# Kernel tuning notes

Hardware: AMD Instinct MI355X
Metric: run time of the kernel (lower is better)

Reference implementation:

```python
import jax, jax.numpy as jnp
import numpy as np

PATCH_SIZES = [4, 8, 16]
B, S, D, H = 32, 1000, 64, 512


def setup_inputs() -> dict:
    key = jax.random.key(0)
    ks = jax.random.split(key, 8)
    inp = {"x": jax.random.normal(ks[0], (B, S, D), dtype=jnp.float32)}
    for i, p in enumerate(PATCH_SIZES):
        fan_in = p * D
        inp[f"W{i}"] = jax.random.normal(ks[1 + 2 * i], (H, fan_in), dtype=jnp.float32) / np.sqrt(fan_in).astype(np.float32)
        inp[f"b{i}"] = jax.random.normal(ks[2 + 2 * i], (H,), dtype=jnp.float32) * 0.01
    inp["pos"] = jax.random.normal(ks[7], (1, 1000, H), dtype=jnp.float32)
    return inp


def reference(x, W0, b0, W1, b1, W2, b2, pos):
    Ws = [W0, W1, W2]
    bs = [b0, b1, b2]
    batch, seq_len, d = x.shape
    min_len = seq_len - max(PATCH_SIZES) + 1  # all scales truncated to this
    embs = []
    for p, W, b in zip(PATCH_SIZES, Ws, bs):
        # sliding windows, stride 1, only the first min_len windows are kept
        idx = jnp.arange(min_len)[:, None] + jnp.arange(p)[None, :]  # (min_len, p)
        win = x[:, idx, :]  # (batch, min_len, p, d) -- im2col gather
        # torch Linear on flattened [time, feature] patch: W[h, t*d + f]
        Wk = W.reshape(-1, p, d)  # (H, p, d)
        embs.append(jnp.einsum('blpd,hpd->blh', win, Wk) + b)
    out = jnp.stack(embs, axis=1).mean(axis=1)  # mean over scales
    return out + pos[:, :min_len, :]
```

## Files before the change

kernel.cpp:

```cpp
#include <hip/hip_runtime.h>
#include <stdint.h>

typedef unsigned short u16;
typedef __attribute__((ext_vector_type(8))) short bf16x8;
typedef __attribute__((ext_vector_type(8))) u16  u16x8;
typedef __attribute__((ext_vector_type(4))) float f32x4;

static constexpr int BATCH  = 32;
static constexpr int SEQ    = 1000;
static constexpr int DIM    = 64;
static constexpr int HOUT   = 512;
static constexpr int MINLEN = 985;
static constexpr int KTOT   = 1024;
static constexpr int AROWS  = 288;

static constexpr size_t XB_OFF   = 0;
static constexpr size_t WF_OFF   = 4u << 20;
static constexpr size_t BE_OFF   = 5u << 20;
static constexpr int    XB_TOTAL = 2048000 + 4096;

__device__ inline u16 f2bf(float f) {
  union { float f; uint32_t u; } v; v.f = f;
  uint32_t r = v.u + 0x7fffu + ((v.u >> 16) & 1u);
  return (u16)(r >> 16);
}

__global__ void pe_prep_x(const float* __restrict__ x, u16* __restrict__ xb) {
  int i = (blockIdx.x * 256 + threadIdx.x) * 8;
  if (i >= XB_TOTAL) return;
  u16x8 o;
  if (i < 2048000) {
    const float4* p = (const float4*)(x + i);
    float4 a = p[0], c = p[1];
    o[0] = f2bf(a.x); o[1] = f2bf(a.y); o[2] = f2bf(a.z); o[3] = f2bf(a.w);
    o[4] = f2bf(c.x); o[5] = f2bf(c.y); o[6] = f2bf(c.z); o[7] = f2bf(c.w);
  } else {
    o = (u16x8)(0);
  }
  *(u16x8*)(xb + i) = o;
}

__global__ void pe_prep_w(const float* __restrict__ W0, const float* __restrict__ W1,
                          const float* __restrict__ W2, const float* __restrict__ b0,
                          const float* __restrict__ b1, const float* __restrict__ b2,
                          u16* __restrict__ Wf, float* __restrict__ beff) {
  int i = blockIdx.x * 256 + threadIdx.x;
  if (i < HOUT * KTOT) {
    int h = i >> 10, j = i & 1023;
    float e = W2[i];
    if (j < 512) e += W1[(h << 9) + j];
    if (j < 256) e += W0[(h << 8) + j];
    Wf[i] = f2bf(e * (1.0f / 3.0f));
  } else if (i < HOUT * KTOT + HOUT) {
    int h = i - HOUT * KTOT;
    beff[h] = (b0[h] + b1[h] + b2[h]) * (1.0f / 3.0f);
  }
}

__device__ inline void gload_lds16(const void* g, void* l) {
  __builtin_amdgcn_global_load_lds(
      (const __attribute__((address_space(1))) uint32_t*)g,
      (__attribute__((address_space(3))) uint32_t*)l, 16, 0, 0);
}

__global__ __launch_bounds__(512, 4) void pe_gemm(
    const u16* __restrict__ xb, const u16* __restrict__ Wf,
    const float* __restrict__ beff, const float* __restrict__ pos,
    float* __restrict__ out) {
  __shared__ u16 ldsA[AROWS * 64];
  __shared__ u16 ldsB[2][128 * 64];

  const int t    = threadIdx.x;
  const int w    = t >> 6;
  const int lane = t & 63;
  const int b    = blockIdx.z;
  const int l0   = blockIdx.y * 256;
  const int n0   = blockIdx.x * 128;
  const int wr   = w >> 1;
  const int wc   = w & 1;
  const int lr   = lane & 15;
  const int g    = lane >> 4;

  const int srow = lane >> 3;
  const int scol = ((lane & 7) ^ (lane >> 3)) * 8;

  const u16* Ab = xb + b * (SEQ * DIM) + l0 * 64;
  const u16* Bb = Wf + (size_t)n0 * KTOT;

  #pragma unroll
  for (int i = 0; i < 4; ++i) {
    int c = w * 4 + i;
    gload_lds16(Ab + (c * 8 + srow) * 64 + scol, &ldsA[c * 512]);
  }
  if (w < 4) {
    int c = 32 + w;
    gload_lds16(Ab + (c * 8 + srow) * 64 + scol, &ldsA[c * 512]);
  }
  #pragma unroll
  for (int i = 0; i < 2; ++i) {
    int c = w * 2 + i;
    gload_lds16(Bb + (size_t)(c * 8 + srow) * KTOT + scol, &ldsB[0][c * 512]);
  }
  __syncthreads();

  f32x4 acc[4][4] = {};
  int cur = 0;

  for (int kt = 0; kt < 16; ++kt) {
    if (kt < 15) {
      #pragma unroll
      for (int i = 0; i < 2; ++i) {
        int c = w * 2 + i;
        gload_lds16(Bb + (size_t)(c * 8 + srow) * KTOT + (kt + 1) * 64 + scol,
                    &ldsB[cur ^ 1][c * 512]);
      }
    }
    #pragma unroll
    for (int kk = 0; kk < 2; ++kk) {
      bf16x8 aF[4], bF[4];
      #pragma unroll
      for (int m = 0; m < 4; ++m) {
        int r = wr * 64 + m * 16 + lr + kt;
        aF[m] = *(const bf16x8*)&ldsA[r * 64 + ((kk * 4 + g) ^ (r & 7)) * 8];
      }
      #pragma unroll
      for (int n = 0; n < 4; ++n) {
        int r = wc * 64 + n * 16 + lr;
        bF[n] = *(const bf16x8*)&ldsB[cur][r * 64 + ((kk * 4 + g) ^ (r & 7)) * 8];
      }
      #pragma unroll
      for (int m = 0; m < 4; ++m)
        #pragma unroll
        for (int n = 0; n < 4; ++n)
          acc[m][n] = __builtin_amdgcn_mfma_f32_16x16x32_bf16(aF[m], bF[n], acc[m][n], 0, 0, 0);
    }
    __syncthreads();
    cur ^= 1;
  }

  #pragma unroll
  for (int n = 0; n < 4; ++n) {
    const int h  = n0 + wc * 64 + n * 16 + lr;
    const float bv = beff[h];
    #pragma unroll
    for (int m = 0; m < 4; ++m) {
      const int rowb = l0 + wr * 64 + m * 16 + (g << 2);
      #pragma unroll
      for (int r = 0; r < 4; ++r) {
        const int l = rowb + r;
        if (l < MINLEN) {
          out[((size_t)b * MINLEN + l) * HOUT + h] =
              acc[m][n][r] + bv + pos[(size_t)l * HOUT + h];
        }
      }
    }
  }
}

extern "C" void kernel_launch(void* const* d_in, const int* in_sizes, int n_in,
                              void* d_out, int out_size, void* d_ws, size_t ws_size,
                              hipStream_t stream) {
  const float* x   = (const float*)d_in[0];
  const float* W0  = (const float*)d_in[1];
  const float* b0  = (const float*)d_in[2];
  const float* W1  = (const float*)d_in[3];
  const float* b1  = (const float*)d_in[4];
  const float* W2  = (const float*)d_in[5];
  const float* b2  = (const float*)d_in[6];
  const float* pos = (const float*)d_in[7];
  float* out = (float*)d_out;

  char* ws  = (char*)d_ws;
  u16*  xbf = (u16*)(ws + XB_OFF);
  u16*  Wf  = (u16*)(ws + WF_OFF);
  float* be = (float*)(ws + BE_OFF);

  hipLaunchKernelGGL(pe_prep_x, dim3(XB_TOTAL / (256 * 8)), dim3(256), 0, stream, x, xbf);
  hipLaunchKernelGGL(pe_prep_w, dim3((HOUT * KTOT + HOUT) / 256), dim3(256), 0, stream,
                     W0, W1, W2, b0, b1, b2, Wf, be);
  hipLaunchKernelGGL(pe_gemm, dim3(HOUT / 128, 4, BATCH), dim3(512), 0, stream,
                     xbf, Wf, be, pos, out);
}
```

Baseline: 58.02 us.

## Widen GEMM N-tile to 256 with triple-buffered B loads and interleaved barriers

Doubles the per-block output tile width from 128 to 256 columns, so each block computes 4x8 MFMA accumulators and the grid shrinks by half. The B operand becomes triple-buffered with a prefetch distance of two k-steps. Global-to-LDS loads are split into quarter chunks interleaved with MFMA phases, using explicit waitcnt/barrier and setprio to overlap memory with compute. This raises reuse of the A (shifted window) tile and hides load latency, at the cost of more registers and LDS, lower occupancy (launch bounds 2), and only 256 blocks on a large-CU GPU.

Measured after the change: 74.47 us. +28.3%, slower.

```diff
diff --git a/kernel.cpp b/kernel.cpp
--- a/kernel.cpp
+++ b/kernel.cpp
@@ -13,6 +13,7 @@
 static constexpr int MINLEN = 985;
 static constexpr int KTOT   = 1024;
 static constexpr int AROWS  = 288;
+static constexpr int BUF    = 256 * 64;
 
 static constexpr size_t XB_OFF   = 0;
 static constexpr size_t WF_OFF   = 4u << 20;
@@ -63,26 +64,26 @@
       (__attribute__((address_space(3))) uint32_t*)l, 16, 0, 0);
 }
 
-__global__ __launch_bounds__(512, 4) void pe_gemm(
+__global__ __launch_bounds__(512, 2) void pe_gemm(
     const u16* __restrict__ xb, const u16* __restrict__ Wf,
     const float* __restrict__ beff, const float* __restrict__ pos,
     float* __restrict__ out) {
   __shared__ u16 ldsA[AROWS * 64];
-  __shared__ u16 ldsB[2][128 * 64];
+  __shared__ u16 ldsB[3 * BUF];
 
   const int t    = threadIdx.x;
   const int w    = t >> 6;
   const int lane = t & 63;
   const int b    = blockIdx.z;
   const int l0   = blockIdx.y * 256;
-  const int n0   = blockIdx.x * 128;
+  const int n0   = blockIdx.x * 256;
   const int wr   = w >> 1;
   const int wc   = w & 1;
   const int lr   = lane & 15;
   const int g    = lane >> 4;
 
   const int srow = lane >> 3;
-  const int scol = ((lane & 7) ^ (lane >> 3)) * 8;
+  const int scol = ((lane & 7) ^ srow) * 8;
 
   const u16* Ab = xb + b * (SEQ * DIM) + l0 * 64;
   const u16* Bb = Wf + (size_t)n0 * KTOT;
@@ -97,50 +98,79 @@
     gload_lds16(Ab + (c * 8 + srow) * 64 + scol, &ldsA[c * 512]);
   }
   #pragma unroll
-  for (int i = 0; i < 2; ++i) {
-    int c = w * 2 + i;
-    gload_lds16(Bb + (size_t)(c * 8 + srow) * KTOT + scol, &ldsB[0][c * 512]);
-  }
-  __syncthreads();
-
-  f32x4 acc[4][4] = {};
-  int cur = 0;
+  for (int i = 0; i < 4; ++i) {
+    int c = w * 4 + i;
+    gload_lds16(Bb + (size_t)(c * 8 + srow) * KTOT + scol, &ldsB[c * 512]);
+  }
+  #pragma unroll
+  for (int i = 0; i < 4; ++i) {
+    int c = w * 4 + i;
+    gload_lds16(Bb + (size_t)(c * 8 + srow) * KTOT + 64 + scol, &ldsB[BUF + c * 512]);
+  }
+  asm volatile("s_waitcnt vmcnt(4)" ::: "memory");
+  __builtin_amdgcn_s_barrier();
+
+  f32x4 acc[4][8] = {};
+  int bc = 0;
+  int bw = 2;
 
   for (int kt = 0; kt < 16; ++kt) {
-    if (kt < 15) {
+    const u16* Bc = &ldsB[bc * BUF];
+    u16* Bw = &ldsB[bw * BUF];
+    const int ksrc = (kt + 2) * 64;
+
+    bf16x8 aF[4], bF[4];
+    #pragma unroll
+    for (int kk = 0; kk < 2; ++kk) {
       #pragma unroll
-      for (int i = 0; i < 2; ++i) {
-        int c = w * 2 + i;
-        gload_lds16(Bb + (size_t)(c * 8 + srow) * KTOT + (kt + 1) * 64 + scol,
-                    &ldsB[cur ^ 1][c * 512]);
+      for (int nh = 0; nh < 2; ++nh) {
+        if (nh == 0) {
+          #pragma unroll
+          for (int m = 0; m < 4; ++m) {
+            int r = wr * 64 + m * 16 + lr + kt;
+            aF[m] = *(const bf16x8*)&ldsA[r * 64 + (((kk * 4 + g) ^ (r & 7)) * 8)];
+          }
+        }
+        #pragma unroll
+        for (int n = 0; n < 4; ++n) {
+          int r = wc * 128 + nh * 64 + n * 16 + lr;
+          bF[n] = *(const bf16x8*)&Bc[r * 64 + (((kk * 4 + g) ^ (r & 7)) * 8)];
+        }
+        if (kt < 14) {
+          int c = w * 4 + (kk * 2 + nh);
+          gload_lds16(Bb + (size_t)(c * 8 + srow) * KTOT + ksrc + scol, Bw + c * 512);
+        }
+        __builtin_amdgcn_s_barrier();
+        asm volatile("s_waitcnt lgkmcnt(0)" ::: "memory");
+        __builtin_amdgcn_sched_barrier(0);
+        __builtin_amdgcn_s_setprio(1);
+        #pragma unroll
+        for (int m = 0; m < 4; ++m)
+          #pragma unroll
+          for (int n = 0; n < 4; ++n)
+            acc[m][nh * 4 + n] =
+                __builtin_amdgcn_mfma_f32_16x16x32_bf16(aF[m], bF[n], acc[m][nh * 4 + n], 0, 0, 0);
+        __builtin_amdgcn_s_setprio(0);
+        if (kk == 1 && nh == 1) {
+          if (kt < 14) {
+            asm volatile("s_waitcnt vmcnt(4)" ::: "memory");
+            __builtin_amdgcn_s_barrier();
+          } else if (kt == 14) {
+            asm volatile("s_waitcnt vmcnt(0)" ::: "memory");
+            __builtin_amdgcn_s_barrier();
+          }
+        } else {
+          __builtin_amdgcn_s_barrier();
+        }
       }
     }
-    #pragma unroll
-    for (int kk = 0; kk < 2; ++kk) {
-      bf16x8 aF[4], bF[4];
-      #pragma unroll
-      for (int m = 0; m < 4; ++m) {
-        int r = wr * 64 + m * 16 + lr + kt;
-        aF[m] = *(const bf16x8*)&ldsA[r * 64 + ((kk * 4 + g) ^ (r & 7)) * 8];
-      }
-      #pragma unroll
-      for (int n = 0; n < 4; ++n) {
-        int r = wc * 64 + n * 16 + lr;
-        bF[n] = *(const bf16x8*)&ldsB[cur][r * 64 + ((kk * 4 + g) ^ (r & 7)) * 8];
-      }
-      #pragma unroll
-      for (int m = 0; m < 4; ++m)
-        #pragma unroll
-        for (int n = 0; n < 4; ++n)
-          acc[m][n] = __builtin_amdgcn_mfma_f32_16x16x32_bf16(aF[m], bF[n], acc[m][n], 0, 0, 0);
-    }
-    __syncthreads();
-    cur ^= 1;
-  }
-
-  #pragma unroll
-  for (int n = 0; n < 4; ++n) {
-    const int h  = n0 + wc * 64 + n * 16 + lr;
+    bc = (bc == 2) ? 0 : bc + 1;
+    bw = (bw == 2) ? 0 : bw + 1;
+  }
+
+  #pragma unroll
+  for (int nj = 0; nj < 8; ++nj) {
+    const int h  = n0 + wc * 128 + nj * 16 + lr;
     const float bv = beff[h];
     #pragma unroll
     for (int m = 0; m < 4; ++m) {
@@ -150,7 +180,7 @@
         const int l = rowb + r;
         if (l < MINLEN) {
           out[((size_t)b * MINLEN + l) * HOUT + h] =
-              acc[m][n][r] + bv + pos[(size_t)l * HOUT + h];
+              acc[m][nj][r] + bv + pos[(size_t)l * HOUT + h];
         }
       }
     }
@@ -178,6 +208,6 @@
   hipLaunchKernelGGL(pe_prep_x, dim3(XB_TOTAL / (256 * 8)), dim3(256), 0, stream, x, xbf);
   hipLaunchKernelGGL(pe_prep_w, dim3((HOUT * KTOT + HOUT) / 256), dim3(256), 0, stream,
                      W0, W1, W2, b0, b1, b2, Wf, be);
-  hipLaunchKernelGGL(pe_gemm, dim3(HOUT / 128, 4, BATCH), dim3(512), 0, stream,
+  hipLaunchKernelGGL(pe_gemm, dim3(HOUT / 256, 4, BATCH), dim3(512), 0, stream,
                      xbf, Wf, be, pos, out);
 }
```

## Merge prep kernels and retile GEMM to 128x256 tiles with 256-thread blocks

Applied to the files above, without the earlier changes.

Merges the x-conversion and weight-fusion prep kernels into one launch, saving a kernel launch. Retiles the GEMM from 256 rows x 128 cols with 8 waves to 128 rows x 256 cols with 4 waves, each wave computing a 64x128 sub-tile. The K step drops to 32 with a new B swizzle, so the loop runs 32 iterations. This raises per-wave register use (32 accumulators) and halves threads per block, trading occupancy for more MFMA work per LDS read.

New measurement: 69.25 us. 1.19x slower.

```diff
diff --git a/kernel.cpp b/kernel.cpp
--- a/kernel.cpp
+++ b/kernel.cpp
@@ -12,7 +12,8 @@
 static constexpr int HOUT   = 512;
 static constexpr int MINLEN = 985;
 static constexpr int KTOT   = 1024;
-static constexpr int AROWS  = 288;
+static constexpr int AROWS  = 144;
+static constexpr int BBUF   = 256 * 32;
 
 static constexpr size_t XB_OFF   = 0;
 static constexpr size_t WF_OFF   = 4u << 20;
@@ -25,35 +26,37 @@
   return (u16)(r >> 16);
 }
 
-__global__ void pe_prep_x(const float* __restrict__ x, u16* __restrict__ xb) {
-  int i = (blockIdx.x * 256 + threadIdx.x) * 8;
-  if (i >= XB_TOTAL) return;
-  u16x8 o;
-  if (i < 2048000) {
-    const float4* p = (const float4*)(x + i);
-    float4 a = p[0], c = p[1];
-    o[0] = f2bf(a.x); o[1] = f2bf(a.y); o[2] = f2bf(a.z); o[3] = f2bf(a.w);
-    o[4] = f2bf(c.x); o[5] = f2bf(c.y); o[6] = f2bf(c.z); o[7] = f2bf(c.w);
+__global__ void pe_prep(const float* __restrict__ x,
+                        const float* __restrict__ W0, const float* __restrict__ W1,
+                        const float* __restrict__ W2, const float* __restrict__ b0,
+                        const float* __restrict__ b1, const float* __restrict__ b2,
+                        u16* __restrict__ xb, u16* __restrict__ Wf,
+                        float* __restrict__ beff) {
+  int bid = blockIdx.x;
+  if (bid < 1002) {
+    int i = (bid * 256 + threadIdx.x) * 8;
+    u16x8 o;
+    if (i < 2048000) {
+      const float4* p = (const float4*)(x + i);
+      float4 a = p[0], c = p[1];
+      o[0] = f2bf(a.x); o[1] = f2bf(a.y); o[2] = f2bf(a.z); o[3] = f2bf(a.w);
+      o[4] = f2bf(c.x); o[5] = f2bf(c.y); o[6] = f2bf(c.z); o[7] = f2bf(c.w);
+    } else {
+      o = (u16x8)(0);
+    }
+    *(u16x8*)(xb + i) = o;
   } else {
-    o = (u16x8)(0);
-  }
-  *(u16x8*)(xb + i) = o;
-}
-
-__global__ void pe_prep_w(const float* __restrict__ W0, const float* __restrict__ W1,
-                          const float* __restrict__ W2, const float* __restrict__ b0,
-                          const float* __restrict__ b1, const float* __restrict__ b2,
-                          u16* __restrict__ Wf, float* __restrict__ beff) {
-  int i = blockIdx.x * 256 + threadIdx.x;
-  if (i < HOUT * KTOT) {
-    int h = i >> 10, j = i & 1023;
-    float e = W2[i];
-    if (j < 512) e += W1[(h << 9) + j];
-    if (j < 256) e += W0[(h << 8) + j];
-    Wf[i] = f2bf(e * (1.0f / 3.0f));
-  } else if (i < HOUT * KTOT + HOUT) {
-    int h = i - HOUT * KTOT;
-    beff[h] = (b0[h] + b1[h] + b2[h]) * (1.0f / 3.0f);
+    int i = (bid - 1002) * 256 + threadIdx.x;
+    if (i < HOUT * KTOT) {
+      int h = i >> 10, j = i & 1023;
+      float e = W2[i];
+      if (j < 512) e += W1[(h << 9) + j];
+      if (j < 256) e += W0[(h << 8) + j];
+      Wf[i] = f2bf(e * (1.0f / 3.0f));
+    } else {
+      int h = i - HOUT * KTOT;
+      beff[h] = (b0[h] + b1[h] + b2[h]) * (1.0f / 3.0f);
+    }
   }
 }
 
@@ -63,26 +66,28 @@
       (__attribute__((address_space(3))) uint32_t*)l, 16, 0, 0);
 }
 
-__global__ __launch_bounds__(512, 4) void pe_gemm(
+__global__ __launch_bounds__(256, 2) void pe_gemm(
     const u16* __restrict__ xb, const u16* __restrict__ Wf,
     const float* __restrict__ beff, const float* __restrict__ pos,
     float* __restrict__ out) {
   __shared__ u16 ldsA[AROWS * 64];
-  __shared__ u16 ldsB[2][128 * 64];
+  __shared__ u16 ldsB[2][BBUF];
 
   const int t    = threadIdx.x;
   const int w    = t >> 6;
   const int lane = t & 63;
   const int b    = blockIdx.z;
-  const int l0   = blockIdx.y * 256;
-  const int n0   = blockIdx.x * 128;
+  const int l0   = blockIdx.y * 128;
+  const int n0   = blockIdx.x * 256;
   const int wr   = w >> 1;
   const int wc   = w & 1;
   const int lr   = lane & 15;
   const int g    = lane >> 4;
 
-  const int srow = lane >> 3;
-  const int scol = ((lane & 7) ^ (lane >> 3)) * 8;
+  const int sra = lane >> 3;
+  const int sca = ((lane & 7) ^ sra) * 8;
+  const int srb = lane >> 2;
+  const int scb = ((lane & 3) ^ ((srb >> 1) & 3)) * 8;
 
   const u16* Ab = xb + b * (SEQ * DIM) + l0 * 64;
   const u16* Bb = Wf + (size_t)n0 * KTOT;
@@ -90,57 +95,57 @@
   #pragma unroll
   for (int i = 0; i < 4; ++i) {
     int c = w * 4 + i;
-    gload_lds16(Ab + (c * 8 + srow) * 64 + scol, &ldsA[c * 512]);
+    gload_lds16(Ab + (c * 8 + sra) * 64 + sca, &ldsA[c * 512]);
   }
-  if (w < 4) {
-    int c = 32 + w;
-    gload_lds16(Ab + (c * 8 + srow) * 64 + scol, &ldsA[c * 512]);
+  if (w < 2) {
+    int c = 16 + w;
+    gload_lds16(Ab + (c * 8 + sra) * 64 + sca, &ldsA[c * 512]);
   }
   #pragma unroll
-  for (int i = 0; i < 2; ++i) {
-    int c = w * 2 + i;
-    gload_lds16(Bb + (size_t)(c * 8 + srow) * KTOT + scol, &ldsB[0][c * 512]);
+  for (int i = 0; i < 4; ++i) {
+    int c = w * 4 + i;
+    gload_lds16(Bb + (size_t)(c * 16 + srb) * KTOT + scb, &ldsB[0][c * 512]);
   }
   __syncthreads();
 
-  f32x4 acc[4][4] = {};
-  int cur = 0;
+  f32x4 acc[4][8] = {};
+  int bc = 0;
 
-  for (int kt = 0; kt < 16; ++kt) {
-    if (kt < 15) {
+  #pragma unroll 2
+  for (int kt = 0; kt < 32; ++kt) {
+    if (kt < 31) {
       #pragma unroll
-      for (int i = 0; i < 2; ++i) {
-        int c = w * 2 + i;
-        gload_lds16(Bb + (size_t)(c * 8 + srow) * KTOT + (kt + 1) * 64 + scol,
-                    &ldsB[cur ^ 1][c * 512]);
+      for (int i = 0; i < 4; ++i) {
+        int c = w * 4 + i;
+        gload_lds16(Bb + (size_t)(c * 16 + srb) * KTOT + (kt + 1) * 32 + scb,
+                    &ldsB[bc ^ 1][c * 512]);
       }
     }
+    bf16x8 aF[4], bF[8];
     #pragma unroll
-    for (int kk = 0; kk < 2; ++kk) {
-      bf16x8 aF[4], bF[4];
+    for (int m = 0; m < 4; ++m) {
+      int r = wr * 64 + m * 16 + lr + (kt >> 1);
+      int s = (((kt & 1) * 4 + g) ^ (r & 7));
+      aF[m] = *(const bf16x8*)&ldsA[r * 64 + s * 8];
+    }
+    #pragma unroll
+    for (int n = 0; n < 8; ++n) {
+      int r = wc * 128 + n * 16 + lr;
+      int s = g ^ ((r >> 1) & 3);
+      bF[n] = *(const bf16x8*)&ldsB[bc][r * 32 + s * 8];
+    }
+    #pragma unroll
+    for (int m = 0; m < 4; ++m)
       #pragma unroll
-      for (int m = 0; m < 4; ++m) {
-        int r = wr * 64 + m * 16 + lr + kt;
-        aF[m] = *(const bf16x8*)&ldsA[r * 64 + ((kk * 4 + g) ^ (r & 7)) * 8];
-      }
-      #pragma unroll
-      for (int n = 0; n < 4; ++n) {
-        int r = wc * 64 + n * 16 + lr;
-        bF[n] = *(const bf16x8*)&ldsB[cur][r * 64 + ((kk * 4 + g) ^ (r & 7)) * 8];
-      }
-      #pragma unroll
-      for (int m = 0; m < 4; ++m)
-        #pragma unroll
-        for (int n = 0; n < 4; ++n)
-          acc[m][n] = __builtin_amdgcn_mfma_f32_16x16x32_bf16(aF[m], bF[n], acc[m][n], 0, 0, 0);
-    }
+      for (int n = 0; n < 8; ++n)
+        acc[m][n] = __builtin_amdgcn_mfma_f32_16x16x32_bf16(aF[m], bF[n], acc[m][n], 0, 0, 0);
     __syncthreads();
-    cur ^= 1;
+    bc ^= 1;
   }
 
   #pragma unroll
-  for (int n = 0; n < 4; ++n) {
-    const int h  = n0 + wc * 64 + n * 16 + lr;
+  for (int nj = 0; nj < 8; ++nj) {
+    const int h  = n0 + wc * 128 + nj * 16 + lr;
     const float bv = beff[h];
     #pragma unroll
     for (int m = 0; m < 4; ++m) {
@@ -150,7 +155,7 @@
         const int l = rowb + r;
         if (l < MINLEN) {
           out[((size_t)b * MINLEN + l) * HOUT + h] =
-              acc[m][n][r] + bv + pos[(size_t)l * HOUT + h];
+              acc[m][nj][r] + bv + pos[(size_t)l * HOUT + h];
         }
       }
     }
@@ -175,9 +180,8 @@
   u16*  Wf  = (u16*)(ws + WF_OFF);
   float* be = (float*)(ws + BE_OFF);
 
-  hipLaunchKernelGGL(pe_prep_x, dim3(XB_TOTAL / (256 * 8)), dim3(256), 0, stream, x, xbf);
-  hipLaunchKernelGGL(pe_prep_w, dim3((HOUT * KTOT + HOUT) / 256), dim3(256), 0, stream,
-                     W0, W1, W2, b0, b1, b2, Wf, be);
-  hipLaunchKernelGGL(pe_gemm, dim3(HOUT / 128, 4, BATCH), dim3(512), 0, stream,
+  hipLaunchKernelGGL(pe_prep, dim3(3052), dim3(256), 0, stream,
+                     x, W0, W1, W2, b0, b1, b2, xbf, Wf, be);
+  hipLaunchKernelGGL(pe_gemm, dim3(HOUT / 256, 8, BATCH), dim3(256), 0, stream,
                      xbf, Wf, be, pos, out);
 }
```
